# Performance work log

Hardware: AMD Instinct MI355X
Metric: run time of the kernel (lower is better)

## Reference

```python
import jax, jax.numpy as jnp
import numpy as np

N_USERS = 100000
N_ITEMS = 50000
N_NODES = N_USERS + N_ITEMS
EMB_DIM = 128
N_LAYERS = 3
NNZ = 2400000
MASK_PROB = 0.2


def setup_inputs() -> dict:
    key = jax.random.key(0)
    ks = jax.random.split(key, 8)
    user_emb = jax.random.normal(ks[0], (N_USERS, EMB_DIM), dtype=jnp.float32) * 0.1
    item_emb = jax.random.normal(ks[1], (N_ITEMS, EMB_DIM), dtype=jnp.float32) * 0.1
    adj_rows = jax.random.randint(ks[2], (NNZ,), 0, N_NODES, dtype=jnp.int32)
    adj_cols = jax.random.randint(ks[3], (NNZ,), 0, N_NODES, dtype=jnp.int32)
    # stand-in for symmetric-normalized adjacency values
    adj_vals = jax.random.uniform(ks[4], (NNZ,), dtype=jnp.float32) * (1.0 / 16.0)
    # deterministic version of mask_embeddings' random binary mask
    mask = (jax.random.uniform(ks[5], (N_USERS, EMB_DIM)) > MASK_PROB).astype(jnp.float32)
    # Dense(emb_dim, relu) params (Glorot-like scale)
    attr_w = jax.random.normal(ks[6], (EMB_DIM, EMB_DIM), dtype=jnp.float32) * (1.0 / np.sqrt(EMB_DIM))
    attr_b = jnp.zeros((EMB_DIM,), dtype=jnp.float32)
    return {"user_emb": user_emb, "item_emb": item_emb, "adj_rows": adj_rows,
            "adj_cols": adj_cols, "adj_vals": adj_vals, "mask": mask,
            "attr_w": attr_w, "attr_b": attr_b}


def _spmm(rows, cols, vals, x):
    # sparse [N,N] @ dense [N,d] via gather + segment_sum
    return jax.ops.segment_sum(vals[:, None] * x[cols], rows, num_segments=N_NODES)


def reference(user_emb, item_emb, adj_rows, adj_cols, adj_vals, mask, attr_w, attr_b):
    alpha = 1.0 / (N_LAYERS + 1)
    all_emb = jnp.concatenate([user_emb, item_emb], axis=0)  # [N, d]
    combined = alpha * all_emb
    for _ in range(N_LAYERS):
        all_emb = _spmm(adj_rows, adj_cols, adj_vals, all_emb)
        combined = combined + alpha * all_emb
    user_final = combined[:N_USERS]
    item_final = combined[N_USERS:]
    masked_user_emb = user_final * mask
    predicted_attributes = jax.nn.relu(masked_user_emb @ attr_w + attr_b)
    return (user_final, item_final, masked_user_emb, predicted_attributes, mask)
```

## Files before the change

### kernel.cpp

```cpp
#include <hip/hip_runtime.h>

#define N_USERS 100000
#define N_ITEMS 50000
#define N_NODES 150000
#define NNZ     2400000
#define ALPHA   0.25f
#define VSCALE  262144.0f
#define VINV    (1.0f / 262144.0f)

static __device__ __forceinline__ unsigned int f2bf(float f) {
    unsigned int u = __float_as_uint(f);
    u += 0x7fffu + ((u >> 16) & 1u);
    return u >> 16;
}
static __device__ __forceinline__ float bflo(unsigned int w) { return __uint_as_float(w << 16); }
static __device__ __forceinline__ float bfhi(unsigned int w) { return __uint_as_float(w & 0xffff0000u); }

__global__ void k_init(const float4* __restrict__ ue, const float4* __restrict__ ie,
                       uint4* __restrict__ x0) {
    int i = blockIdx.x * 256 + threadIdx.x;
    if (i >= N_NODES * 16) return;
    float4 a, b;
    if (i < N_USERS * 16) { a = ue[2 * i]; b = ue[2 * i + 1]; }
    else { int k = i - N_USERS * 16; a = ie[2 * k]; b = ie[2 * k + 1]; }
    uint4 o;
    o.x = f2bf(a.x) | (f2bf(a.y) << 16);
    o.y = f2bf(a.z) | (f2bf(a.w) << 16);
    o.z = f2bf(b.x) | (f2bf(b.y) << 16);
    o.w = f2bf(b.z) | (f2bf(b.w) << 16);
    x0[i] = o;
}

__global__ void k_histrank(const int* __restrict__ rows, int* __restrict__ cnt,
                           int* __restrict__ rank) {
    int stride = gridDim.x * blockDim.x;
    for (int i = blockIdx.x * blockDim.x + threadIdx.x; i < NNZ; i += stride)
        rank[i] = atomicAdd(&cnt[rows[i]], 1);
}

__global__ void k_scan1(const int* __restrict__ cnt, int* __restrict__ tmp, int* __restrict__ part) {
    __shared__ int sm[1024];
    int g = blockIdx.x * 1024 + threadIdx.x;
    int v = (g < N_NODES) ? cnt[g] : 0;
    sm[threadIdx.x] = v;
    __syncthreads();
    for (int off = 1; off < 1024; off <<= 1) {
        int t = (threadIdx.x >= off) ? sm[threadIdx.x - off] : 0;
        __syncthreads();
        sm[threadIdx.x] += t;
        __syncthreads();
    }
    if (g < N_NODES) tmp[g] = sm[threadIdx.x];
    if (threadIdx.x == 1023) part[blockIdx.x] = sm[1023];
}

__global__ void k_scan2(int* __restrict__ part, int n) {
    __shared__ int sm[256];
    int v = (threadIdx.x < n) ? part[threadIdx.x] : 0;
    sm[threadIdx.x] = v;
    __syncthreads();
    for (int off = 1; off < 256; off <<= 1) {
        int t = (threadIdx.x >= off) ? sm[threadIdx.x - off] : 0;
        __syncthreads();
        sm[threadIdx.x] += t;
        __syncthreads();
    }
    if (threadIdx.x < n) part[threadIdx.x] = sm[threadIdx.x];
}

__global__ void k_scan3(const int* __restrict__ tmp, const int* __restrict__ part, int* __restrict__ rp) {
    int g = blockIdx.x * 1024 + threadIdx.x;
    if (g < N_NODES) {
        int add = blockIdx.x ? part[blockIdx.x - 1] : 0;
        rp[g + 1] = tmp[g] + add;
    }
    if (g == 0) rp[0] = 0;
}

__launch_bounds__(256)
__global__ void k_scatter(const int* __restrict__ rows, const int* __restrict__ cols,
                          const float* __restrict__ vals, const int* __restrict__ rank,
                          const int* __restrict__ rp, unsigned int* __restrict__ ev) {
    int cls = blockIdx.x & 7;
    int base = (blockIdx.x >> 3) * 256 + threadIdx.x;
    for (int i = base; i < NNZ; i += 65536) {
        int r = rows[i];
        if (((r >> 11) & 7) != cls) continue;
        int v14 = (int)(vals[i] * VSCALE + 0.5f);
        v14 = min(v14, 16383);
        unsigned int w = ((unsigned int)cols[i] << 14) | (unsigned int)v14;
        ev[rp[r] + rank[i]] = w;
    }
}

__launch_bounds__(256)
__global__ void k_spmm(const int* __restrict__ rp, const unsigned int* __restrict__ ev,
                       const unsigned short* __restrict__ x, unsigned short* __restrict__ y) {
    int r = blockIdx.x * 4 + (threadIdx.x >> 6);
    if (r >= N_NODES) return;
    int l = (threadIdx.x & 63) * 2;
    const unsigned short* xp = x + l;
    float ax = 0.f, ay = 0.f;
    int s = rp[r], e = rp[r + 1];
    int j = s;
    for (; j + 4 <= e; j += 4) {
        unsigned int m0 = ev[j], m1 = ev[j + 1], m2 = ev[j + 2], m3 = ev[j + 3];
        unsigned int w0 = *(const unsigned int*)(xp + (m0 >> 14) * 128);
        unsigned int w1 = *(const unsigned int*)(xp + (m1 >> 14) * 128);
        unsigned int w2 = *(const unsigned int*)(xp + (m2 >> 14) * 128);
        unsigned int w3 = *(const unsigned int*)(xp + (m3 >> 14) * 128);
        float v0 = (m0 & 16383u) * VINV, v1 = (m1 & 16383u) * VINV;
        float v2 = (m2 & 16383u) * VINV, v3 = (m3 & 16383u) * VINV;
        ax += v0 * bflo(w0) + v1 * bflo(w1) + v2 * bflo(w2) + v3 * bflo(w3);
        ay += v0 * bfhi(w0) + v1 * bfhi(w1) + v2 * bfhi(w2) + v3 * bfhi(w3);
    }
    for (; j < e; ++j) {
        unsigned int m = ev[j];
        unsigned int w = *(const unsigned int*)(xp + (m >> 14) * 128);
        float v = (m & 16383u) * VINV;
        ax += v * bflo(w);
        ay += v * bfhi(w);
    }
    unsigned int o = f2bf(ax) | (f2bf(ay) << 16);
    *(unsigned int*)(y + r * 128 + l) = o;
}

__global__ void k_combine(const float4* __restrict__ ue, const float4* __restrict__ ie,
                          const unsigned short* __restrict__ y1, const unsigned short* __restrict__ y2,
                          const unsigned short* __restrict__ y3, float4* __restrict__ comb) {
    int i = blockIdx.x * 256 + threadIdx.x;
    if (i >= N_NODES * 32) return;
    float4 e = (i < N_USERS * 32) ? ue[i] : ie[i - N_USERS * 32];
    uint2 a = *(const uint2*)(y1 + i * 4);
    uint2 b = *(const uint2*)(y2 + i * 4);
    uint2 c = *(const uint2*)(y3 + i * 4);
    float4 o;
    o.x = ALPHA * (e.x + bflo(a.x) + bflo(b.x) + bflo(c.x));
    o.y = ALPHA * (e.y + bfhi(a.x) + bfhi(b.x) + bfhi(c.x));
    o.z = ALPHA * (e.z + bflo(a.y) + bflo(b.y) + bflo(c.y));
    o.w = ALPHA * (e.w + bfhi(a.y) + bfhi(b.y) + bfhi(c.y));
    comb[i] = o;
}

__launch_bounds__(256)
__global__ void k_mmfused(const float* __restrict__ comb, const float* __restrict__ mask,
                          const float* __restrict__ W, const float* __restrict__ b,
                          float* __restrict__ masked, float* __restrict__ maskO,
                          float* __restrict__ pred) {
    __shared__ float Wl[128 * 128];
    float4* W4s = (float4*)Wl;
    const float4* W4g = (const float4*)W;
    for (int i = threadIdx.x; i < 4096; i += 256) W4s[i] = W4g[i];
    __syncthreads();

    int rowt = threadIdx.x >> 3;
    int colg = threadIdx.x & 7;
    int row  = blockIdx.x * 32 + rowt;

    const float4* cu4 = (const float4*)comb;
    const float4* mk4 = (const float4*)mask;
    float4* m4  = (float4*)masked;
    float4* mo4 = (float4*)maskO;
    #pragma unroll
    for (int jj = 0; jj < 4; ++jj) {
        int idx = row * 32 + colg + 8 * jj;
        float4 u = cu4[idx], m = mk4[idx];
        float4 r = make_float4(u.x * m.x, u.y * m.y, u.z * m.z, u.w * m.w);
        m4[idx]  = r;
        mo4[idx] = m;
    }

    const float* cr = comb + row * 128;
    const float* mr = mask + row * 128;
    float4 a0 = make_float4(0, 0, 0, 0), a1 = a0, a2 = a0, a3 = a0;
    for (int k = 0; k < 128; ++k) {
        float av = cr[k] * mr[k];
        float4 w0 = W4s[k * 32 + colg];
        float4 w1 = W4s[k * 32 + colg + 8];
        float4 w2 = W4s[k * 32 + colg + 16];
        float4 w3 = W4s[k * 32 + colg + 24];
        a0.x += av * w0.x; a0.y += av * w0.y; a0.z += av * w0.z; a0.w += av * w0.w;
        a1.x += av * w1.x; a1.y += av * w1.y; a1.z += av * w1.z; a1.w += av * w1.w;
        a2.x += av * w2.x; a2.y += av * w2.y; a2.z += av * w2.z; a2.w += av * w2.w;
        a3.x += av * w3.x; a3.y += av * w3.y; a3.z += av * w3.z; a3.w += av * w3.w;
    }
    const float4* b4 = (const float4*)b;
    float4* out4 = (float4*)pred;
    float4 acc[4] = {a0, a1, a2, a3};
    #pragma unroll
    for (int jj = 0; jj < 4; ++jj) {
        float4 bb = b4[colg + 8 * jj];
        float4 r;
        r.x = fmaxf(acc[jj].x + bb.x, 0.f);
        r.y = fmaxf(acc[jj].y + bb.y, 0.f);
        r.z = fmaxf(acc[jj].z + bb.z, 0.f);
        r.w = fmaxf(acc[jj].w + bb.w, 0.f);
        out4[row * 32 + colg + 8 * jj] = r;
    }
}

extern "C" void kernel_launch(void* const* d_in, const int* in_sizes, int n_in,
                              void* d_out, int out_size, void* d_ws, size_t ws_size,
                              hipStream_t stream) {
    const float* ue     = (const float*)d_in[0];
    const float* ie     = (const float*)d_in[1];
    const int*   arows  = (const int*)d_in[2];
    const int*   acols  = (const int*)d_in[3];
    const float* avals  = (const float*)d_in[4];
    const float* mask   = (const float*)d_in[5];
    const float* attr_w = (const float*)d_in[6];
    const float* attr_b = (const float*)d_in[7];
    float* out = (float*)d_out;

    float* comb   = out;
    float* masked = out + 19200000;
    float* pred   = out + 32000000;
    float* maskO  = out + 44800000;

    unsigned short* x0b = (unsigned short*)(out + 19200000);
    unsigned short* y1  = (unsigned short*)(out + 28800000);
    unsigned short* y2  = (unsigned short*)(out + 38400000);
    unsigned short* y3  = (unsigned short*)(out + 48000000);

    char* ws = (char*)d_ws;
    int*          rank = (int*)         (ws);
    unsigned int* ev   = (unsigned int*)(ws +  9600000);
    int*          cnt  = (int*)         (ws + 19200000);
    int*          rp   = (int*)         (ws + 19800064);
    int*          tmp  = (int*)         (ws + 20400128);
    int*          part = (int*)         (ws + 21000192);

    hipMemsetAsync(cnt, 0, (N_NODES + 1) * sizeof(int), stream);
    k_init<<<9375, 256, 0, stream>>>((const float4*)ue, (const float4*)ie, (uint4*)x0b);
    k_histrank<<<2048, 256, 0, stream>>>(arows, cnt, rank);
    k_scan1<<<147, 1024, 0, stream>>>(cnt, tmp, part);
    k_scan2<<<1, 256, 0, stream>>>(part, 147);
    k_scan3<<<147, 1024, 0, stream>>>(tmp, part, rp);
    k_scatter<<<2048, 256, 0, stream>>>(arows, acols, avals, rank, rp, ev);

    k_spmm<<<37500, 256, 0, stream>>>(rp, ev, x0b, y1);
    k_spmm<<<37500, 256, 0, stream>>>(rp, ev, y1, y2);
    k_spmm<<<37500, 256, 0, stream>>>(rp, ev, y2, y3);

    k_combine<<<18750, 256, 0, stream>>>((const float4*)ue, (const float4*)ie,
                                         y1, y2, y3, (float4*)comb);
    k_mmfused<<<3125, 256, 0, stream>>>(comb, mask, attr_w, attr_b, masked, maskO, pred);
}
```

Measured before the change: 915.3 us.

## Fuse final SpMM layer with combine and masking, add XCD block swizzle

```diff
diff --git a/kernel.cpp b/kernel.cpp
--- a/kernel.cpp
+++ b/kernel.cpp
@@ -15,6 +15,11 @@
 }
 static __device__ __forceinline__ float bflo(unsigned int w) { return __uint_as_float(w << 16); }
 static __device__ __forceinline__ float bfhi(unsigned int w) { return __uint_as_float(w & 0xffff0000u); }
+
+static __device__ __forceinline__ int xcd_swz(int orig, int q, int rem) {
+    int xcd = orig & 7, idx = orig >> 3;
+    return (xcd < rem ? xcd * (q + 1) : rem * (q + 1) + (xcd - rem) * q) + idx;
+}
 
 __global__ void k_init(const float4* __restrict__ ue, const float4* __restrict__ ie,
                        uint4* __restrict__ x0) {
@@ -96,7 +101,8 @@
 __launch_bounds__(256)
 __global__ void k_spmm(const int* __restrict__ rp, const unsigned int* __restrict__ ev,
                        const unsigned short* __restrict__ x, unsigned short* __restrict__ y) {
-    int r = blockIdx.x * 4 + (threadIdx.x >> 6);
+    int b = xcd_swz(blockIdx.x, 4687, 4);
+    int r = b * 4 + __builtin_amdgcn_readfirstlane(threadIdx.x >> 6);
     if (r >= N_NODES) return;
     int l = (threadIdx.x & 63) * 2;
     const unsigned short* xp = x + l;
@@ -125,28 +131,56 @@
     *(unsigned int*)(y + r * 128 + l) = o;
 }
 
-__global__ void k_combine(const float4* __restrict__ ue, const float4* __restrict__ ie,
-                          const unsigned short* __restrict__ y1, const unsigned short* __restrict__ y2,
-                          const unsigned short* __restrict__ y3, float4* __restrict__ comb) {
-    int i = blockIdx.x * 256 + threadIdx.x;
-    if (i >= N_NODES * 32) return;
-    float4 e = (i < N_USERS * 32) ? ue[i] : ie[i - N_USERS * 32];
-    uint2 a = *(const uint2*)(y1 + i * 4);
-    uint2 b = *(const uint2*)(y2 + i * 4);
-    uint2 c = *(const uint2*)(y3 + i * 4);
-    float4 o;
-    o.x = ALPHA * (e.x + bflo(a.x) + bflo(b.x) + bflo(c.x));
-    o.y = ALPHA * (e.y + bfhi(a.x) + bfhi(b.x) + bfhi(c.x));
-    o.z = ALPHA * (e.z + bflo(a.y) + bflo(b.y) + bflo(c.y));
-    o.w = ALPHA * (e.w + bfhi(a.y) + bfhi(b.y) + bfhi(c.y));
-    comb[i] = o;
-}
-
-__launch_bounds__(256)
-__global__ void k_mmfused(const float* __restrict__ comb, const float* __restrict__ mask,
-                          const float* __restrict__ W, const float* __restrict__ b,
-                          float* __restrict__ masked, float* __restrict__ maskO,
-                          float* __restrict__ pred) {
+__launch_bounds__(256)
+__global__ void k_spmm3(const int* __restrict__ rp, const unsigned int* __restrict__ ev,
+                        const unsigned short* __restrict__ y2src,
+                        const unsigned short* __restrict__ y1,
+                        const float2* __restrict__ ue2, const float2* __restrict__ ie2,
+                        const float2* __restrict__ mask2,
+                        float2* __restrict__ comb2, float2* __restrict__ masked2,
+                        float2* __restrict__ maskO2) {
+    int b = xcd_swz(blockIdx.x, 4687, 4);
+    int r = b * 4 + __builtin_amdgcn_readfirstlane(threadIdx.x >> 6);
+    if (r >= N_NODES) return;
+    int l = threadIdx.x & 63;
+    const unsigned short* xp = y2src + 2 * l;
+    float ax = 0.f, ay = 0.f;
+    int s = rp[r], e = rp[r + 1];
+    int j = s;
+    for (; j + 4 <= e; j += 4) {
+        unsigned int m0 = ev[j], m1 = ev[j + 1], m2 = ev[j + 2], m3 = ev[j + 3];
+        unsigned int w0 = *(const unsigned int*)(xp + (m0 >> 14) * 128);
+        unsigned int w1 = *(const unsigned int*)(xp + (m1 >> 14) * 128);
+        unsigned int w2 = *(const unsigned int*)(xp + (m2 >> 14) * 128);
+        unsigned int w3 = *(const unsigned int*)(xp + (m3 >> 14) * 128);
+        float v0 = (m0 & 16383u) * VINV, v1 = (m1 & 16383u) * VINV;
+        float v2 = (m2 & 16383u) * VINV, v3 = (m3 & 16383u) * VINV;
+        ax += v0 * bflo(w0) + v1 * bflo(w1) + v2 * bflo(w2) + v3 * bflo(w3);
+        ay += v0 * bfhi(w0) + v1 * bfhi(w1) + v2 * bfhi(w2) + v3 * bfhi(w3);
+    }
+    for (; j < e; ++j) {
+        unsigned int m = ev[j];
+        unsigned int w = *(const unsigned int*)(xp + (m >> 14) * 128);
+        float v = (m & 16383u) * VINV;
+        ax += v * bflo(w);
+        ay += v * bfhi(w);
+    }
+    float2 em = (r < N_USERS) ? ue2[r * 64 + l] : ie2[(r - N_USERS) * 64 + l];
+    unsigned int a1 = *(const unsigned int*)(y1    + r * 128 + 2 * l);
+    unsigned int a2 = *(const unsigned int*)(y2src + r * 128 + 2 * l);
+    float cx = ALPHA * (em.x + bflo(a1) + bflo(a2) + ax);
+    float cy = ALPHA * (em.y + bfhi(a1) + bfhi(a2) + ay);
+    comb2[r * 64 + l] = make_float2(cx, cy);
+    if (r < N_USERS) {
+        float2 m = mask2[r * 64 + l];
+        masked2[r * 64 + l] = make_float2(cx * m.x, cy * m.y);
+        maskO2[r * 64 + l]  = m;
+    }
+}
+
+__launch_bounds__(256)
+__global__ void k_mm(const float* __restrict__ A, const float* __restrict__ W,
+                     const float* __restrict__ b, float* __restrict__ pred) {
     __shared__ float Wl[128 * 128];
     float4* W4s = (float4*)Wl;
     const float4* W4g = (const float4*)W;
@@ -156,25 +190,11 @@
     int rowt = threadIdx.x >> 3;
     int colg = threadIdx.x & 7;
     int row  = blockIdx.x * 32 + rowt;
-
-    const float4* cu4 = (const float4*)comb;
-    const float4* mk4 = (const float4*)mask;
-    float4* m4  = (float4*)masked;
-    float4* mo4 = (float4*)maskO;
-    #pragma unroll
-    for (int jj = 0; jj < 4; ++jj) {
-        int idx = row * 32 + colg + 8 * jj;
-        float4 u = cu4[idx], m = mk4[idx];
-        float4 r = make_float4(u.x * m.x, u.y * m.y, u.z * m.z, u.w * m.w);
-        m4[idx]  = r;
-        mo4[idx] = m;
-    }
-
-    const float* cr = comb + row * 128;
-    const float* mr = mask + row * 128;
+    const float* ar = A + row * 128;
+
     float4 a0 = make_float4(0, 0, 0, 0), a1 = a0, a2 = a0, a3 = a0;
     for (int k = 0; k < 128; ++k) {
-        float av = cr[k] * mr[k];
+        float av = ar[k];
         float4 w0 = W4s[k * 32 + colg];
         float4 w1 = W4s[k * 32 + colg + 8];
         float4 w2 = W4s[k * 32 + colg + 16];
@@ -217,18 +237,16 @@
     float* pred   = out + 32000000;
     float* maskO  = out + 44800000;
 
-    unsigned short* x0b = (unsigned short*)(out + 19200000);
-    unsigned short* y1  = (unsigned short*)(out + 28800000);
-    unsigned short* y2  = (unsigned short*)(out + 38400000);
-    unsigned short* y3  = (unsigned short*)(out + 48000000);
-
     char* ws = (char*)d_ws;
-    int*          rank = (int*)         (ws);
-    unsigned int* ev   = (unsigned int*)(ws +  9600000);
-    int*          cnt  = (int*)         (ws + 19200000);
-    int*          rp   = (int*)         (ws + 19800064);
-    int*          tmp  = (int*)         (ws + 20400128);
-    int*          part = (int*)         (ws + 21000192);
+    unsigned short* x0b  = (unsigned short*)(ws);
+    unsigned short* y1   = (unsigned short*)(ws +  38400000);
+    unsigned short* y2   = (unsigned short*)(ws +  76800000);
+    int*            rank = (int*)          (ws + 115200000);
+    unsigned int*   ev   = (unsigned int*) (ws + 124800000);
+    int*            cnt  = (int*)          (ws + 134400000);
+    int*            rp   = (int*)          (ws + 135000064);
+    int*            tmp  = (int*)          (ws + 135600128);
+    int*            part = (int*)          (ws + 136200192);
 
     hipMemsetAsync(cnt, 0, (N_NODES + 1) * sizeof(int), stream);
     k_init<<<9375, 256, 0, stream>>>((const float4*)ue, (const float4*)ie, (uint4*)x0b);
@@ -240,9 +258,10 @@
 
     k_spmm<<<37500, 256, 0, stream>>>(rp, ev, x0b, y1);
     k_spmm<<<37500, 256, 0, stream>>>(rp, ev, y1, y2);
-    k_spmm<<<37500, 256, 0, stream>>>(rp, ev, y2, y3);
-
-    k_combine<<<18750, 256, 0, stream>>>((const float4*)ue, (const float4*)ie,
-                                         y1, y2, y3, (float4*)comb);
-    k_mmfused<<<3125, 256, 0, stream>>>(comb, mask, attr_w, attr_b, masked, maskO, pred);
-}
+    k_spmm3<<<37500, 256, 0, stream>>>(rp, ev, y2, y1,
+                                       (const float2*)ue, (const float2*)ie,
+                                       (const float2*)mask,
+                                       (float2*)comb, (float2*)masked, (float2*)maskO);
+
+    k_mm<<<3125, 256, 0, stream>>>(masked, attr_w, attr_b, pred);
+}
```

After: 886.3 us. 1.03x faster.
